# Kernel tuning notes

Measured on AMD Instinct MI355X. Metric: run time of the kernel, lower is better.

Reference implementation:

```python
import jax, jax.numpy as jnp
import numpy as np

# Static module config (must match init_kwargs / input_specs)
C, HEADS, POINTS, LEVELS = 256, 8, 8, 2
H, W = 128, 128           # BEV grid per agent/level
NQ = H * W                # num_query = H*W
DH = C // HEADS           # per-head dim


def setup_inputs() -> dict:
    key = jax.random.key(0)
    ks = jax.random.split(key, 12)
    s = 0.02
    return {
        "query": jax.random.normal(ks[0], (1, NQ, C), jnp.float32),
        "query_pos": jax.random.normal(ks[1], (1, NQ, C), jnp.float32),
        "value": jax.random.normal(ks[2], (LEVELS, NQ, C), jnp.float32),
        "reference_points": jax.random.uniform(ks[3], (1, NQ, LEVELS, 2), jnp.float32),
        "spatial_shapes": jnp.full((LEVELS, 2), H, dtype=jnp.int32),
        "W_off": jax.random.normal(ks[4], (C, LEVELS * HEADS * POINTS * 2), jnp.float32) * s,
        "b_off": jax.random.normal(ks[5], (LEVELS * HEADS * POINTS * 2,), jnp.float32) * s,
        "W_attn": jax.random.normal(ks[6], (C, LEVELS * HEADS * POINTS), jnp.float32) * s,
        "b_attn": jax.random.normal(ks[7], (LEVELS * HEADS * POINTS,), jnp.float32) * s,
        "W_val": jax.random.normal(ks[8], (C, C), jnp.float32) * s,
        "b_val": jax.random.normal(ks[9], (C,), jnp.float32) * s,
        "W_out": jax.random.normal(ks[10], (C, C), jnp.float32) * s,
        "b_out": jax.random.normal(ks[11], (C,), jnp.float32) * s,
    }


def _bilinear(img, x, y):
    """grid_sample-style bilinear, align_corners=False, zero padding.
    img: (H, W, D); x, y: (...) pixel-space coords. Returns (..., D)."""
    Hh, Ww = img.shape[0], img.shape[1]
    x0f, y0f = jnp.floor(x), jnp.floor(y)
    x0, y0 = x0f.astype(jnp.int32), y0f.astype(jnp.int32)
    x1, y1 = x0 + 1, y0 + 1
    wx1, wy1 = x - x0f, y - y0f
    wx0, wy0 = 1.0 - wx1, 1.0 - wy1

    def gather(yy, xx):
        valid = (yy >= 0) & (yy < Hh) & (xx >= 0) & (xx < Ww)
        g = img[jnp.clip(yy, 0, Hh - 1), jnp.clip(xx, 0, Ww - 1)]
        return jnp.where(valid[..., None], g, 0.0)

    return (gather(y0, x0) * (wy0 * wx0)[..., None]
            + gather(y0, x1) * (wy0 * wx1)[..., None]
            + gather(y1, x0) * (wy1 * wx0)[..., None]
            + gather(y1, x1) * (wy1 * wx1)[..., None])


_sample_heads = jax.vmap(_bilinear, in_axes=(0, 0, 0))  # over heads


def reference(query, query_pos, value, reference_points, spatial_shapes,
              W_off, b_off, W_attn, b_attn, W_val, b_val, W_out, b_out):
    identity = query                                        # (1, NQ, C)
    q = (query + query_pos)[0]                              # (NQ, C), bs=1

    v = value @ W_val + b_val                               # (L, NQ, C)
    v = v.reshape(LEVELS, H, W, HEADS, DH)                  # per-level feature maps

    off = (q @ W_off + b_off).reshape(NQ, HEADS, LEVELS, POINTS, 2)
    attn = (q @ W_attn + b_attn).reshape(NQ, HEADS, LEVELS * POINTS)
    attn = jax.nn.softmax(attn, axis=-1).reshape(NQ, HEADS, LEVELS, POINTS)

    # offset_normalizer = (W, H) per level
    norm = jnp.stack([spatial_shapes[:, 1], spatial_shapes[:, 0]], -1).astype(q.dtype)  # (L, 2)
    # sampling_locations in normalized [0,1] coords: (NQ, HEADS, LEVELS, POINTS, 2)
    loc = reference_points[0][:, None, :, None, :] + off / norm[None, None, :, None, :]

    out = jnp.zeros((NQ, HEADS, DH), dtype=q.dtype)
    for l in range(LEVELS):
        img_l = jnp.transpose(v[l], (2, 0, 1, 3))           # (HEADS, H, W, DH)
        # align_corners=False: px = x_norm * W - 0.5
        xl = jnp.transpose(loc[:, :, l, :, 0], (1, 0, 2)) * W - 0.5  # (HEADS, NQ, POINTS)
        yl = jnp.transpose(loc[:, :, l, :, 1], (1, 0, 2)) * H - 0.5
        sampled = _sample_heads(img_l, xl, yl)              # (HEADS, NQ, POINTS, DH)
        out = out + jnp.einsum('hqpd,qhp->qhd', sampled, attn[:, :, l, :])

    out = out.reshape(NQ, C) @ W_out + b_out                # (NQ, C)
    return out[None] + identity                             # dropout is identity (eval / p=0)
```

## Files before the change

### kernel.cpp

```cpp
#include <hip/hip_runtime.h>
#include <hip/hip_bf16.h>
#include <math.h>

#define NQ     16384
#define CDIM   256
#define NHEADS 8
#define NPTS   8
#define NLVL   2
#define HH     128
#define WWID   128
#define DHEAD  32
#define NCAT   384

#define PW        130
#define CELLB     32
#define ROWB      (PW * CELLB)
#define MAPB      (PW * PW * CELLB)
#define BORDER_BLKS 16
#define TRANS_BLKS  224

typedef __bf16 bf16_t;
typedef __bf16 bf16x8 __attribute__((ext_vector_type(8)));
typedef float  f32x4  __attribute__((ext_vector_type(4)));
typedef float  f32x2  __attribute__((ext_vector_type(2)));

typedef __attribute__((address_space(1))) const uint32_t gau32;
typedef __attribute__((address_space(3))) uint32_t lau32;

__device__ __forceinline__ bf16_t f2b(float f) { return (bf16_t)f; }

__device__ __forceinline__ bf16x8 cvt8(float4 a, float4 b) {
    bf16x8 v;
    v[0] = f2b(a.x); v[1] = f2b(a.y); v[2] = f2b(a.z); v[3] = f2b(a.w);
    v[4] = f2b(b.x); v[5] = f2b(b.y); v[6] = f2b(b.z); v[7] = f2b(b.w);
    return v;
}

__global__ __launch_bounds__(256) void prep_k(const float* __restrict__ W_val,
                                              const float* __restrict__ W_off,
                                              const float* __restrict__ W_attn,
                                              const float* __restrict__ W_out,
                                              unsigned char* __restrict__ v2,
                                              bf16_t* __restrict__ Wt_val,
                                              bf16_t* __restrict__ Wt_qa,
                                              bf16_t* __restrict__ Wt_out) {
    const int b = blockIdx.x;
    if (b < BORDER_BLKS) {
        unsigned char* map = v2 + (size_t)b * MAPB;
        for (int i = threadIdx.x; i < 516; i += 256) {
            int y, x;
            if (i < 130)      { y = 0;        x = i;       }
            else if (i < 260) { y = 129;      x = i - 130; }
            else if (i < 388) { y = i - 259;  x = 0;       }
            else              { y = i - 387;  x = 129;     }
            uint4* p = reinterpret_cast<uint4*>(map + (size_t)y * ROWB + x * CELLB);
            p[0] = make_uint4(0, 0, 0, 0);
            p[1] = make_uint4(0, 0, 0, 0);
        }
        return;
    }
    {
        const int tb = b - BORDER_BLKS;
        const float* W; bf16_t* Wt; int N, t; bool permute = false;
        if (tb < 64)       { W = W_val;  Wt = Wt_val;            N = 256; t = tb;       permute = true; }
        else if (tb < 128) { W = W_off;  Wt = Wt_qa;             N = 256; t = tb - 64;  }
        else if (tb < 160) { W = W_attn; Wt = Wt_qa + 256 * 256; N = 128; t = tb - 128; }
        else               { W = W_out;  Wt = Wt_out;            N = 256; t = tb - 160; }
        const int ntn = N >> 5;
        const int k0 = (t / ntn) * 32, n0 = (t % ntn) * 32;
        const int tx = threadIdx.x & 31, ty = threadIdx.x >> 5;
        __shared__ float s[32][33];
#pragma unroll
        for (int i = 0; i < 4; ++i)
            s[ty + 8 * i][tx] = W[(size_t)(k0 + ty + 8 * i) * N + n0 + tx];
        __syncthreads();
#pragma unroll
        for (int i = 0; i < 4; ++i) {
            const int n = n0 + ty + 8 * i;
            const int p = permute ? ((n & ~63) | ((n & 3) << 4) | ((n & 63) >> 2)) : n;
            Wt[(size_t)p * 256 + k0 + tx] = f2b(s[tx][ty + 8 * i]);
        }
    }
}

template <int AMODE, bool OUT_BF16, bool ADD_SRC, bool PERM_V>
__device__ __forceinline__ void gemm_body(bf16_t (&As)[128][64], bf16_t (&Bs)[128][64],
                                          int bidx, int bidy,
                                          const bf16_t* __restrict__ Abf,
                                          const float* __restrict__ Af0,
                                          const float* __restrict__ Af1,
                                          const bf16_t* __restrict__ Bt,
                                          const float* __restrict__ bias,
                                          const float* __restrict__ bias2,
                                          int Nsplit,
                                          const float* __restrict__ addsrc,
                                          void* __restrict__ Cout,
                                          int N, int K) {
    const int tid  = threadIdx.x;
    const int wave = tid >> 6;
    const int lane = tid & 63;
    const int rowBase = bidy * 128;
    const int colBase = bidx * 128;
    const int wm = (wave & 1) * 64;
    const int wn = (wave >> 1) * 64;
    const int fr = lane & 15;
    const int fq = lane >> 4;

    f32x4 acc[4][4] = {};

    const int lrow = lane >> 3;
    const int scol = ((lane & 7) ^ lrow) * 8;

    for (int k0 = 0; k0 < K; k0 += 64) {
        __syncthreads();
        float4 ra[4][2], rb[4][2];
        if constexpr (AMODE == 0) {
#pragma unroll
            for (int t = 0; t < 4; ++t) {
                const bf16_t* src =
                    Abf + (size_t)(rowBase + wave * 32 + t * 8 + lrow) * K + k0 + scol;
                __builtin_amdgcn_global_load_lds((gau32*)src,
                                                 (lau32*)&As[wave * 32 + t * 8][0],
                                                 16, 0, 0);
            }
        } else {
#pragma unroll
            for (int t = 0; t < 4; ++t) {
                const float* src =
                    Af0 + (size_t)(rowBase + wave * 32 + t * 8 + lrow) * K + k0 + scol;
                ra[t][0] = *reinterpret_cast<const float4*>(src);
                ra[t][1] = *reinterpret_cast<const float4*>(src + 4);
            }
            if constexpr (AMODE == 2) {
#pragma unroll
                for (int t = 0; t < 4; ++t) {
                    const float* src =
                        Af1 + (size_t)(rowBase + wave * 32 + t * 8 + lrow) * K + k0 + scol;
                    rb[t][0] = *reinterpret_cast<const float4*>(src);
                    rb[t][1] = *reinterpret_cast<const float4*>(src + 4);
                }
            }
        }
#pragma unroll
        for (int t = 0; t < 4; ++t) {
            const bf16_t* src =
                Bt + (size_t)(colBase + wave * 32 + t * 8 + lrow) * K + k0 + scol;
            __builtin_amdgcn_global_load_lds((gau32*)src,
                                             (lau32*)&Bs[wave * 32 + t * 8][0],
                                             16, 0, 0);
        }
        if constexpr (AMODE != 0) {
#pragma unroll
            for (int t = 0; t < 4; ++t) {
                float4 a = ra[t][0], c = ra[t][1];
                if constexpr (AMODE == 2) {
                    a.x += rb[t][0].x; a.y += rb[t][0].y;
                    a.z += rb[t][0].z; a.w += rb[t][0].w;
                    c.x += rb[t][1].x; c.y += rb[t][1].y;
                    c.z += rb[t][1].z; c.w += rb[t][1].w;
                }
                *reinterpret_cast<bf16x8*>(
                    &As[wave * 32 + t * 8 + lrow][(lane & 7) * 8]) = cvt8(a, c);
            }
        }
        __syncthreads();
#pragma unroll
        for (int ks = 0; ks < 2; ++ks) {
            const int gk = ((ks * 4 + fq) ^ (fr & 7)) * 8;
            bf16x8 af[4], bfr[4];
#pragma unroll
            for (int i = 0; i < 4; ++i)
                af[i] = *reinterpret_cast<const bf16x8*>(&As[wm + i * 16 + fr][gk]);
#pragma unroll
            for (int j = 0; j < 4; ++j)
                bfr[j] = *reinterpret_cast<const bf16x8*>(&Bs[wn + j * 16 + fr][gk]);
#pragma unroll
            for (int i = 0; i < 4; ++i)
#pragma unroll
                for (int j = 0; j < 4; ++j)
                    acc[i][j] = __builtin_amdgcn_mfma_f32_16x16x32_bf16(af[i], bfr[j],
                                                                        acc[i][j], 0, 0, 0);
        }
    }

    if (PERM_V) {
        const int lbase = colBase + wn + fr * 4;
        const float bv0 = bias[lbase], bv1 = bias[lbase + 1];
        const float bv2 = bias[lbase + 2], bv3 = bias[lbase + 3];
        const int hh = (lbase >> 5) & 7;
        const int dbase = lbase & 31;
        unsigned char* outp = (unsigned char*)Cout;
#pragma unroll
        for (int i = 0; i < 4; ++i) {
#pragma unroll
            for (int r = 0; r < 4; ++r) {
                const int row = rowBase + wm + i * 16 + fq * 4 + r;
                const int lv = row >> 14, cell = row & 16383;
                const int y = cell >> 7, x = cell & 127;
                uint32_t pk = __builtin_amdgcn_cvt_pk_fp8_f32(
                    acc[i][0][r] + bv0, acc[i][1][r] + bv1, 0, false);
                pk = (uint32_t)__builtin_amdgcn_cvt_pk_fp8_f32(
                    acc[i][2][r] + bv2, acc[i][3][r] + bv3, pk, true);
                *reinterpret_cast<uint32_t*>(
                    outp + (size_t)(lv * NHEADS + hh) * MAPB
                         + (size_t)(y + 1) * ROWB + (x + 1) * CELLB + dbase) = pk;
            }
        }
        return;
    }

#pragma unroll
    for (int j = 0; j < 4; ++j) {
        const int col = colBase + wn + j * 16 + fr;
        const float bv = (col < Nsplit) ? bias[col] : bias2[col - Nsplit];
#pragma unroll
        for (int i = 0; i < 4; ++i) {
#pragma unroll
            for (int r = 0; r < 4; ++r) {
                const int row = rowBase + wm + i * 16 + fq * 4 + r;
                float vv = acc[i][j][r] + bv;
                if (ADD_SRC) vv += addsrc[(size_t)row * N + col];
                if (OUT_BF16)
                    ((bf16_t*)Cout)[(size_t)row * N + col] = f2b(vv);
                else
                    ((float*)Cout)[(size_t)row * N + col] = vv;
            }
        }
    }
}

__global__ __launch_bounds__(256, 3) void fused_proj_k(const float* __restrict__ value,
                                                       const float* __restrict__ query,
                                                       const float* __restrict__ query_pos,
                                                       const bf16_t* __restrict__ Wt_val,
                                                       const bf16_t* __restrict__ Wt_qa,
                                                       const float* __restrict__ b_val,
                                                       const float* __restrict__ b_off,
                                                       const float* __restrict__ b_attn,
                                                       unsigned char* __restrict__ v2,
                                                       bf16_t* __restrict__ cbuf) {
    __shared__ __align__(16) bf16_t As[128][64];
    __shared__ __align__(16) bf16_t Bs[128][64];
    const int b = blockIdx.x;
    if (b < 512) {
        const int bidy = (b >> 4) * 8 + (b & 7);
        const int bidx = (b >> 3) & 1;
        gemm_body<1, true, false, true>(As, Bs, bidx, bidy, nullptr, value, nullptr,
                                        Wt_val, b_val, b_val, 256, nullptr, v2,
                                        CDIM, CDIM);
    } else {
        const int b2 = b - 512;
        const int bidy = (b2 / 24) * 8 + (b2 & 7);
        const int bidx = (b2 >> 3) % 3;
        gemm_body<2, true, false, false>(As, Bs, bidx, bidy, nullptr, query, query_pos,
                                         Wt_qa, b_off, b_attn, 256, nullptr, cbuf,
                                         NCAT, CDIM);
    }
}

__global__ __launch_bounds__(256, 3) void outproj_k(const bf16_t* __restrict__ tmp,
                                                    const bf16_t* __restrict__ Wt_out,
                                                    const float* __restrict__ b_out,
                                                    const float* __restrict__ query,
                                                    float* __restrict__ out) {
    __shared__ __align__(16) bf16_t As[128][64];
    __shared__ __align__(16) bf16_t Bs[128][64];
    const int b = blockIdx.x;
    const int bidy = (b >> 4) * 8 + (b & 7);
    const int bidx = (b >> 3) & 1;
    gemm_body<0, false, true, false>(As, Bs, bidx, bidy, tmp, nullptr, nullptr,
                                     Wt_out, b_out, b_out, 256, query, out,
                                     CDIM, CDIM);
}

__device__ __forceinline__ void acc_tap4(uint4 u, float w, f32x2* acc2) {
    acc2[0] += __builtin_amdgcn_cvt_pk_f32_fp8((int)u.x, false) * w;
    acc2[1] += __builtin_amdgcn_cvt_pk_f32_fp8((int)u.x, true)  * w;
    acc2[2] += __builtin_amdgcn_cvt_pk_f32_fp8((int)u.y, false) * w;
    acc2[3] += __builtin_amdgcn_cvt_pk_f32_fp8((int)u.y, true)  * w;
    acc2[4] += __builtin_amdgcn_cvt_pk_f32_fp8((int)u.z, false) * w;
    acc2[5] += __builtin_amdgcn_cvt_pk_f32_fp8((int)u.z, true)  * w;
    acc2[6] += __builtin_amdgcn_cvt_pk_f32_fp8((int)u.w, false) * w;
    acc2[7] += __builtin_amdgcn_cvt_pk_f32_fp8((int)u.w, true)  * w;
}

__global__ __launch_bounds__(256) void sample_k(const unsigned char* __restrict__ v2,
                                                const bf16_t* __restrict__ cbuf,
                                                const float* __restrict__ refp,
                                                bf16_t* __restrict__ tmp) {
    const int b    = blockIdx.x;
    const int h    = b & 7;
    const int qblk = b >> 3;
    const int tid  = threadIdx.x;
    const int qloc = tid >> 1;
    const int ck   = tid & 1;
    const int q    = qblk * 128 + qloc;

    const bf16_t* qrow = cbuf + (size_t)q * NCAT;
    const float4 rp = *reinterpret_cast<const float4*>(refp + (size_t)q * 4);

    const bf16_t* attp = qrow + 256 + h * 16;
    bf16x8 A0 = *reinterpret_cast<const bf16x8*>(attp);
    bf16x8 A1 = *reinterpret_cast<const bf16x8*>(attp + 8);
    float e[16];
#pragma unroll
    for (int i = 0; i < 8; ++i) { e[i] = (float)A0[i]; e[8 + i] = (float)A1[i]; }
    float m = e[0];
#pragma unroll
    for (int i = 1; i < 16; ++i) m = fmaxf(m, e[i]);
    float s = 0.f;
#pragma unroll
    for (int i = 0; i < 16; ++i) { e[i] = __expf(e[i] - m); s += e[i]; }
    const float inv = 1.f / s;
#pragma unroll
    for (int i = 0; i < 16; ++i) e[i] *= inv;

    f32x2 acc2[8] = {};

#pragma unroll
    for (int l = 0; l < NLVL; ++l) {
        const float bx = (l == 0 ? rp.x : rp.z) * (float)WWID - 0.5f;
        const float by = (l == 0 ? rp.y : rp.w) * (float)HH - 0.5f;
        const unsigned char* base = v2 + (size_t)(l * NHEADS + h) * MAPB
                                       + 131 * CELLB + ck * 16;
        const bf16_t* offp = qrow + h * 32 + l * 16;
        bf16x8 o0 = *reinterpret_cast<const bf16x8*>(offp);
        bf16x8 o1 = *reinterpret_cast<const bf16x8*>(offp + 8);
        float ox[8], oy[8];
#pragma unroll
        for (int i = 0; i < 4; ++i) {
            ox[i]     = (float)o0[2 * i];  oy[i]     = (float)o0[2 * i + 1];
            ox[4 + i] = (float)o1[2 * i];  oy[4 + i] = (float)o1[2 * i + 1];
        }

#pragma unroll
        for (int p = 0; p < NPTS; ++p) {
            const float px = bx + ox[p];
            const float py = by + oy[p];
            const float w  = e[l * 8 + p];
            const float x0f = floorf(px), y0f = floorf(py);
            const int x0 = (int)x0f, y0 = (int)y0f;
            const float wx1 = px - x0f, wy1 = py - y0f;
            const float wx0 = 1.f - wx1, wy0 = 1.f - wy1;
            const int x0c = min(max(x0, -1), 128);
            const int x1c = min(max(x0 + 1, -1), 128);
            const int y0c = min(max(y0, -1), 128);
            const int y1c = min(max(y0 + 1, -1), 128);
            const unsigned char* r0 = base + y0c * ROWB;
            const unsigned char* r1 = base + y1c * ROWB;
            uint4 u00 = *reinterpret_cast<const uint4*>(r0 + x0c * CELLB);
            uint4 u10 = *reinterpret_cast<const uint4*>(r0 + x1c * CELLB);
            uint4 u01 = *reinterpret_cast<const uint4*>(r1 + x0c * CELLB);
            uint4 u11 = *reinterpret_cast<const uint4*>(r1 + x1c * CELLB);
            const float wy0w = w * wy0, wy1w = w * wy1;
            acc_tap4(u00, wy0w * wx0, acc2);
            acc_tap4(u10, wy0w * wx1, acc2);
            acc_tap4(u01, wy1w * wx0, acc2);
            acc_tap4(u11, wy1w * wx1, acc2);
        }
    }

    bf16x8 ov0, ov1;
#pragma unroll
    for (int i = 0; i < 4; ++i) {
        ov0[2 * i]     = f2b(acc2[i].x);
        ov0[2 * i + 1] = f2b(acc2[i].y);
        ov1[2 * i]     = f2b(acc2[4 + i].x);
        ov1[2 * i + 1] = f2b(acc2[4 + i].y);
    }
    bf16_t* op = tmp + (size_t)q * CDIM + h * DHEAD + ck * 16;
    *reinterpret_cast<bf16x8*>(op)     = ov0;
    *reinterpret_cast<bf16x8*>(op + 8) = ov1;
}

extern "C" void kernel_launch(void* const* d_in, const int* in_sizes, int n_in,
                              void* d_out, int out_size, void* d_ws, size_t ws_size,
                              hipStream_t stream) {
    const float* query     = (const float*)d_in[0];
    const float* query_pos = (const float*)d_in[1];
    const float* value     = (const float*)d_in[2];
    const float* refp      = (const float*)d_in[3];
    const float* W_off  = (const float*)d_in[5];
    const float* b_off  = (const float*)d_in[6];
    const float* W_attn = (const float*)d_in[7];
    const float* b_attn = (const float*)d_in[8];
    const float* W_val  = (const float*)d_in[9];
    const float* b_val  = (const float*)d_in[10];
    const float* W_out  = (const float*)d_in[11];
    const float* b_out  = (const float*)d_in[12];
    float* out = (float*)d_out;

    char* ws = (char*)d_ws;
    unsigned char* v2 = (unsigned char*)(ws);
    bf16_t* cbuf    = (bf16_t*)(ws + 8654848);
    bf16_t* tmp     = (bf16_t*)(ws + 21237760);
    bf16_t* Wt_val  = (bf16_t*)(ws + 29626368);
    bf16_t* Wt_qa   = (bf16_t*)(ws + 29757440);
    bf16_t* Wt_out  = (bf16_t*)(ws + 29954048);

    prep_k<<<BORDER_BLKS + TRANS_BLKS, 256, 0, stream>>>(
        W_val, W_off, W_attn, W_out, v2, Wt_val, Wt_qa, Wt_out);
    fused_proj_k<<<896, 256, 0, stream>>>(value, query, query_pos,
                                          Wt_val, Wt_qa, b_val, b_off, b_attn,
                                          v2, cbuf);
    sample_k<<<1024, 256, 0, stream>>>(v2, cbuf, refp, tmp);
    outproj_k<<<256, 256, 0, stream>>>(tmp, Wt_out, b_out, query, out);
}
```

Before: 181.5 us.

## Double-buffer GEMM LDS tiles to overlap next-tile loads with MFMA

Converts the shared GEMM body to a two-stage LDS ping-pong. The next K-tile's global loads (async global_load_lds for bf16, register prefetch for fp32 A) are issued before the current tile's MFMAs, which removes one barrier per iteration. This is meant to hide global memory latency behind compute. In exchange, LDS use doubles to 64KB per block and launch bounds drop from 3 to 2 blocks per CU, so occupancy falls. K is only 256 (4 tiles), which limits how much overlap is available.

```diff
diff --git a/kernel.cpp b/kernel.cpp
--- a/kernel.cpp
+++ b/kernel.cpp
@@ -84,7 +84,7 @@
 }
 
 template <int AMODE, bool OUT_BF16, bool ADD_SRC, bool PERM_V>
-__device__ __forceinline__ void gemm_body(bf16_t (&As)[128][64], bf16_t (&Bs)[128][64],
+__device__ __forceinline__ void gemm_body(bf16_t (&As)[2][128][64], bf16_t (&Bs)[2][128][64],
                                           int bidx, int bidy,
                                           const bf16_t* __restrict__ Abf,
                                           const float* __restrict__ Af0,
@@ -110,76 +110,97 @@
 
     const int lrow = lane >> 3;
     const int scol = ((lane & 7) ^ lrow) * 8;
-
-    for (int k0 = 0; k0 < K; k0 += 64) {
-        __syncthreads();
-        float4 ra[4][2], rb[4][2];
+    const int nt = K >> 6;
+
+    float4 ra[4][2], rb[4][2];
+
+    auto issueA = [&](int t, int buf) {
         if constexpr (AMODE == 0) {
 #pragma unroll
-            for (int t = 0; t < 4; ++t) {
+            for (int tt = 0; tt < 4; ++tt) {
                 const bf16_t* src =
-                    Abf + (size_t)(rowBase + wave * 32 + t * 8 + lrow) * K + k0 + scol;
+                    Abf + (size_t)(rowBase + wave * 32 + tt * 8 + lrow) * K + t * 64 + scol;
                 __builtin_amdgcn_global_load_lds((gau32*)src,
-                                                 (lau32*)&As[wave * 32 + t * 8][0],
+                                                 (lau32*)&As[buf][wave * 32 + tt * 8][0],
                                                  16, 0, 0);
             }
         } else {
 #pragma unroll
-            for (int t = 0; t < 4; ++t) {
+            for (int tt = 0; tt < 4; ++tt) {
                 const float* src =
-                    Af0 + (size_t)(rowBase + wave * 32 + t * 8 + lrow) * K + k0 + scol;
-                ra[t][0] = *reinterpret_cast<const float4*>(src);
-                ra[t][1] = *reinterpret_cast<const float4*>(src + 4);
+                    Af0 + (size_t)(rowBase + wave * 32 + tt * 8 + lrow) * K + t * 64 + scol;
+                ra[tt][0] = *reinterpret_cast<const float4*>(src);
+                ra[tt][1] = *reinterpret_cast<const float4*>(src + 4);
             }
             if constexpr (AMODE == 2) {
 #pragma unroll
-                for (int t = 0; t < 4; ++t) {
+                for (int tt = 0; tt < 4; ++tt) {
                     const float* src =
-                        Af1 + (size_t)(rowBase + wave * 32 + t * 8 + lrow) * K + k0 + scol;
-                    rb[t][0] = *reinterpret_cast<const float4*>(src);
-                    rb[t][1] = *reinterpret_cast<const float4*>(src + 4);
+                        Af1 + (size_t)(rowBase + wave * 32 + tt * 8 + lrow) * K + t * 64 + scol;
+                    rb[tt][0] = *reinterpret_cast<const float4*>(src);
+                    rb[tt][1] = *reinterpret_cast<const float4*>(src + 4);
                 }
             }
         }
-#pragma unroll
-        for (int t = 0; t < 4; ++t) {
+    };
+    auto issueB = [&](int t, int buf) {
+#pragma unroll
+        for (int tt = 0; tt < 4; ++tt) {
             const bf16_t* src =
-                Bt + (size_t)(colBase + wave * 32 + t * 8 + lrow) * K + k0 + scol;
+                Bt + (size_t)(colBase + wave * 32 + tt * 8 + lrow) * K + t * 64 + scol;
             __builtin_amdgcn_global_load_lds((gau32*)src,
-                                             (lau32*)&Bs[wave * 32 + t * 8][0],
+                                             (lau32*)&Bs[buf][wave * 32 + tt * 8][0],
                                              16, 0, 0);
         }
+    };
+    auto writeA = [&](int buf) {
         if constexpr (AMODE != 0) {
 #pragma unroll
-            for (int t = 0; t < 4; ++t) {
-                float4 a = ra[t][0], c = ra[t][1];
+            for (int tt = 0; tt < 4; ++tt) {
+                float4 a = ra[tt][0], c = ra[tt][1];
                 if constexpr (AMODE == 2) {
-                    a.x += rb[t][0].x; a.y += rb[t][0].y;
-                    a.z += rb[t][0].z; a.w += rb[t][0].w;
-                    c.x += rb[t][1].x; c.y += rb[t][1].y;
-                    c.z += rb[t][1].z; c.w += rb[t][1].w;
+                    a.x += rb[tt][0].x; a.y += rb[tt][0].y;
+                    a.z += rb[tt][0].z; a.w += rb[tt][0].w;
+                    c.x += rb[tt][1].x; c.y += rb[tt][1].y;
+                    c.z += rb[tt][1].z; c.w += rb[tt][1].w;
                 }
                 *reinterpret_cast<bf16x8*>(
-                    &As[wave * 32 + t * 8 + lrow][(lane & 7) * 8]) = cvt8(a, c);
-            }
-        }
-        __syncthreads();
+                    &As[buf][wave * 32 + tt * 8 + lrow][(lane & 7) * 8]) = cvt8(a, c);
+            }
+        }
+    };
+
+    issueA(0, 0);
+    issueB(0, 0);
+    writeA(0);
+    __syncthreads();
+
+    for (int t = 0; t < nt; ++t) {
+        const int c = t & 1, n = c ^ 1;
+        if (t + 1 < nt) {
+            issueA(t + 1, n);
+            issueB(t + 1, n);
+        }
 #pragma unroll
         for (int ks = 0; ks < 2; ++ks) {
             const int gk = ((ks * 4 + fq) ^ (fr & 7)) * 8;
             bf16x8 af[4], bfr[4];
 #pragma unroll
             for (int i = 0; i < 4; ++i)
-                af[i] = *reinterpret_cast<const bf16x8*>(&As[wm + i * 16 + fr][gk]);
+                af[i] = *reinterpret_cast<const bf16x8*>(&As[c][wm + i * 16 + fr][gk]);
 #pragma unroll
             for (int j = 0; j < 4; ++j)
-                bfr[j] = *reinterpret_cast<const bf16x8*>(&Bs[wn + j * 16 + fr][gk]);
+                bfr[j] = *reinterpret_cast<const bf16x8*>(&Bs[c][wn + j * 16 + fr][gk]);
 #pragma unroll
             for (int i = 0; i < 4; ++i)
 #pragma unroll
                 for (int j = 0; j < 4; ++j)
                     acc[i][j] = __builtin_amdgcn_mfma_f32_16x16x32_bf16(af[i], bfr[j],
                                                                         acc[i][j], 0, 0, 0);
+        }
+        if (t + 1 < nt) {
+            writeA(n);
+            __syncthreads();
         }
     }
 
@@ -229,7 +250,7 @@
     }
 }
 
-__global__ __launch_bounds__(256, 3) void fused_proj_k(const float* __restrict__ value,
+__global__ __launch_bounds__(256, 2) void fused_proj_k(const float* __restrict__ value,
                                                        const float* __restrict__ query,
                                                        const float* __restrict__ query_pos,
                                                        const bf16_t* __restrict__ Wt_val,
@@ -239,8 +260,8 @@
                                                        const float* __restrict__ b_attn,
                                                        unsigned char* __restrict__ v2,
                                                        bf16_t* __restrict__ cbuf) {
-    __shared__ __align__(16) bf16_t As[128][64];
-    __shared__ __align__(16) bf16_t Bs[128][64];
+    __shared__ __align__(16) bf16_t As[2][128][64];
+    __shared__ __align__(16) bf16_t Bs[2][128][64];
     const int b = blockIdx.x;
     if (b < 512) {
         const int bidy = (b >> 4) * 8 + (b & 7);
@@ -258,13 +279,13 @@
     }
 }
 
-__global__ __launch_bounds__(256, 3) void outproj_k(const bf16_t* __restrict__ tmp,
+__global__ __launch_bounds__(256, 2) void outproj_k(const bf16_t* __restrict__ tmp,
                                                     const bf16_t* __restrict__ Wt_out,
                                                     const float* __restrict__ b_out,
                                                     const float* __restrict__ query,
                                                     float* __restrict__ out) {
-    __shared__ __align__(16) bf16_t As[128][64];
-    __shared__ __align__(16) bf16_t Bs[128][64];
+    __shared__ __align__(16) bf16_t As[2][128][64];
+    __shared__ __align__(16) bf16_t Bs[2][128][64];
     const int b = blockIdx.x;
     const int bidy = (b >> 4) * 8 + (b & 7);
     const int bidx = (b >> 3) & 1;
```

After: 177.8 us. 1.02x faster.
